# Kernel tuning notes

Measured on AMD Instinct MI355X. Metric: run time of the kernel, lower is better.

## Reference

```python
import jax, jax.numpy as jnp
import numpy as np

SEQ_LEN, BATCH, NUM_GROUPS, GROUP = 12, 512, 16, 32
H, E, MLP, BOTTLE, PRE = 128, 64, 1024, 1024, 512


def _pool_net(h, pos, num_groups, Wp, bp, W1, b1, W2, b2):
    # PoolHiddenNet: for each scene group, pairwise relative positions -> MLP -> max over neighbors
    B = h.shape[0]
    G = B // num_groups
    hg = h.reshape(num_groups, G, -1)          # (NG, G, H)
    pg = pos.reshape(num_groups, G, 2)         # (NG, G, 2)
    rel = pg[:, None, :, :] - pg[:, :, None, :]  # [g,i,j] = pos_j - pos_i
    emb = rel @ Wp.T + bp                      # (NG, G, G, E)
    hj = jnp.broadcast_to(hg[:, None, :, :], (num_groups, G, G, hg.shape[-1]))
    feats = jnp.concatenate([emb, hj], axis=-1)  # (NG, G, G, E+H)
    x = jax.nn.relu(feats @ W1.T + b1)         # (NG, G, G, 512)
    x = jax.nn.relu(x @ W2.T + b2)             # (NG, G, G, 1024)
    return x.max(axis=2).reshape(B, -1)        # max over neighbors j


def setup_inputs() -> dict:
    key = jax.random.key(0)
    ks = jax.random.split(key, 24)
    s = 0.05
    starts = np.arange(NUM_GROUPS, dtype=np.int64) * GROUP
    seq_start_end = jnp.asarray(np.stack([starts, starts + GROUP], axis=1))
    return {
        "last_pos": jax.random.normal(ks[0], (BATCH, 2), jnp.float32),
        "last_pos_rel": jax.random.normal(ks[1], (BATCH, 2), jnp.float32),
        "hh": jax.random.normal(ks[2], (1, BATCH, H), jnp.float32),
        "ch": jax.random.normal(ks[3], (1, BATCH, H), jnp.float32),
        "pred_traj_rel": jax.random.normal(ks[4], (SEQ_LEN, BATCH, 2), jnp.float32),
        "seq_start_end": seq_start_end,
        # LSTM (torch layout: gates ordered i,f,g,o)
        "W_ih": jax.random.normal(ks[5], (4 * H, E), jnp.float32) * s,
        "W_hh": jax.random.normal(ks[6], (4 * H, H), jnp.float32) * s,
        "b_ih": jax.random.normal(ks[7], (4 * H,), jnp.float32) * s,
        "b_hh": jax.random.normal(ks[8], (4 * H,), jnp.float32) * s,
        # spatial_embedding Linear(2, E)
        "Wse": jax.random.normal(ks[9], (E, 2), jnp.float32) * s,
        "bse": jax.random.normal(ks[10], (E,), jnp.float32) * s,
        # hidden2pos Linear(H, 2)
        "Wpos": jax.random.normal(ks[11], (2, H), jnp.float32) * s,
        "bpos": jax.random.normal(ks[12], (2,), jnp.float32) * s,
        # pool_net spatial_embedding Linear(2, E)
        "Wp": jax.random.normal(ks[13], (E, 2), jnp.float32) * s,
        "bp": jax.random.normal(ks[14], (E,), jnp.float32) * s,
        # pool_net mlp_pre_pool: [E+H, 512, BOTTLE], relu after each linear
        "W1": jax.random.normal(ks[15], (PRE, E + H), jnp.float32) * s,
        "b1": jax.random.normal(ks[16], (PRE,), jnp.float32) * s,
        "W2": jax.random.normal(ks[17], (BOTTLE, PRE), jnp.float32) * s,
        "b2": jax.random.normal(ks[18], (BOTTLE,), jnp.float32) * s,
        # decoder mlp: [H+BOTTLE, MLP, H], relu after each linear
        "Wm1": jax.random.normal(ks[19], (MLP, H + BOTTLE), jnp.float32) * s,
        "bm1": jax.random.normal(ks[20], (MLP,), jnp.float32) * s,
        "Wm2": jax.random.normal(ks[21], (H, MLP), jnp.float32) * s,
        "bm2": jax.random.normal(ks[22], (H,), jnp.float32) * s,
    }


def reference(last_pos, last_pos_rel, hh, ch, pred_traj_rel, seq_start_end,
              W_ih, W_hh, b_ih, b_hh, Wse, bse, Wpos, bpos,
              Wp, bp, W1, b1, W2, b2, Wm1, bm1, Wm2, bm2):
    num_groups = seq_start_end.shape[0]
    h0, c0 = hh[0], ch[0]
    dec_in0 = last_pos_rel @ Wse.T + bse

    def step(carry, gt_rel):
        last_pos_c, h, c, dec_in, loss = carry
        # single-layer LSTM cell (torch gate order i,f,g,o)
        gates = dec_in @ W_ih.T + b_ih + h @ W_hh.T + b_hh
        i, f, g, o = jnp.split(gates, 4, axis=-1)
        c = jax.nn.sigmoid(f) * c + jax.nn.sigmoid(i) * jnp.tanh(g)
        h = jax.nn.sigmoid(o) * jnp.tanh(c)
        rel_pos = h @ Wpos.T + bpos
        curr_pos = rel_pos + last_pos_c
        # pool every timestep + mlp back down to h_dim, replaces hidden state
        pool_h = _pool_net(h, curr_pos, num_groups, Wp, bp, W1, b1, W2, b2)
        dh = jnp.concatenate([h, pool_h], axis=1)
        dh = jax.nn.relu(dh @ Wm1.T + bm1)
        h = jax.nn.relu(dh @ Wm2.T + bm2)
        # training mode: teacher forcing + MSE loss
        loss = loss + jnp.mean((rel_pos - gt_rel) ** 2)
        dec_in = gt_rel @ Wse.T + bse
        return (curr_pos, h, c, dec_in, loss), rel_pos

    init = (last_pos, h0, c0, dec_in0, jnp.float32(0.0))
    (_, _, _, _, loss), pred_traj = jax.lax.scan(step, init, pred_traj_rel)
    return pred_traj, loss
```

## Files before the change

kernel.cpp:

```cpp
#include <hip/hip_runtime.h>
#include <math.h>

#define BATCH 512
#define NG 16
#define GSZ 32
#define H 128
#define E 64
#define PRE 512
#define BOT 1024
#define MLPD 1024
#define SEQ 12
#define AK 1152

typedef __attribute__((ext_vector_type(8))) short bf16x8;
typedef __attribute__((ext_vector_type(4))) float f32x4;

union bf8pack { ushort s[8]; uint4 v; };

__device__ __forceinline__ unsigned short f2bf(float f) {
    unsigned u = __float_as_uint(f);
    u += 0x7FFF + ((u >> 16) & 1);
    return (unsigned short)(u >> 16);
}

__device__ __forceinline__ uint4 pack8(const float* s) {
    float4 a = *(const float4*)s, b = *(const float4*)(s + 4);
    bf8pack o;
    o.s[0] = f2bf(a.x); o.s[1] = f2bf(a.y); o.s[2] = f2bf(a.z); o.s[3] = f2bf(a.w);
    o.s[4] = f2bf(b.x); o.s[5] = f2bf(b.y); o.s[6] = f2bf(b.z); o.s[7] = f2bf(b.w);
    return o.v;
}

#define GLB(p) ((const __attribute__((address_space(1))) unsigned int*)(p))
#define LDS(p) ((__attribute__((address_space(3))) unsigned int*)(p))

#define U0 ((BOT * PRE) / 8)
#define U1 ((MLPD * AK) / 8)
#define U2 ((H * MLPD) / 8)
#define U3 ((PRE * H) / 8)
#define U4 (PRE)
#define U5 ((BATCH * H) / 4)
#define U5b ((BATCH * H) / 8)
#define U6 (BATCH * 2)
#define U7 ((512 * 128) / 8)
#define U8 (512)
#define PREP_TOT (U0 + U1 + U2 + U3 + U4 + U5 + U5b + U6 + U7 + U8 + 1)

__global__ void prep_kernel(
    const float* __restrict__ W2, const float* __restrict__ Wm1,
    const float* __restrict__ Wm2, const float* __restrict__ W1,
    const float* __restrict__ Wp, const float* __restrict__ bp, const float* __restrict__ b1,
    const float* __restrict__ ch, const float* __restrict__ hh, const float* __restrict__ last_pos,
    const float* __restrict__ Wih, const float* __restrict__ Whh,
    const float* __restrict__ bih, const float* __restrict__ bhh,
    const float* __restrict__ Wse, const float* __restrict__ bse,
    unsigned short* __restrict__ W2pk, unsigned short* __restrict__ Wm1pk,
    unsigned short* __restrict__ Wm2pk, unsigned short* __restrict__ W1pk,
    float* __restrict__ Wcx, float* __restrict__ Wcy, float* __restrict__ biash,
    float* __restrict__ cbuf, unsigned short* __restrict__ Ahpk, float* __restrict__ pos,
    unsigned short* __restrict__ Whpk,
    float* __restrict__ Wx0, float* __restrict__ Wx1, float* __restrict__ bx,
    float* __restrict__ loss)
{
    long idx = (long)blockIdx.x * 256 + threadIdx.x;
    if (idx < U0) {
        int u = (int)idx;
        int lane = u & 63, rest = u >> 6;
        int ksg = rest & 15, cg = rest >> 4;
        int col = cg * 16 + (lane & 15);
        int kk = ksg * 32 + (lane >> 4) * 8;
        *(uint4*)&W2pk[(size_t)u * 8] = pack8(&W2[(size_t)col * PRE + kk]);
        return;
    }
    idx -= U0;
    if (idx < U1) {
        int u = (int)idx;
        int lane = u & 63, rest = u >> 6;
        int ksg = rest % 36, cg = rest / 36;
        int col = cg * 16 + (lane & 15);
        int k = ksg * 32 + (lane >> 4) * 8;
        *(uint4*)&Wm1pk[(size_t)u * 8] = pack8(&Wm1[(size_t)col * AK + k]);
        return;
    }
    idx -= U1;
    if (idx < U2) {
        int u = (int)idx;
        int lane = u & 63, rest = u >> 6;
        int ksg = rest & 31, cg = rest >> 5;
        int col = cg * 16 + (lane & 15);
        int k = ksg * 32 + (lane >> 4) * 8;
        *(uint4*)&Wm2pk[(size_t)u * 8] = pack8(&Wm2[(size_t)col * MLPD + k]);
        return;
    }
    idx -= U2;
    if (idx < U3) {
        int u = (int)idx;
        int l16 = u & 15, quad = (u >> 4) & 3, nt = (u >> 6) & 3, ks = (u >> 8) & 3, w = u >> 10;
        int col = w * 64 + nt * 16 + l16;
        int k = ks * 32 + quad * 8;
        *(uint4*)&W1pk[(size_t)u * 8] = pack8(&W1[col * 192 + E + k]);
        return;
    }
    idx -= U3;
    if (idx < U4) {
        int p = (int)idx;
        float sx = 0.f, sy = 0.f, sb = 0.f;
#pragma unroll 8
        for (int e = 0; e < E; ++e) {
            float w = W1[p * 192 + e];
            sx += w * Wp[e * 2 + 0];
            sy += w * Wp[e * 2 + 1];
            sb += w * bp[e];
        }
        Wcx[p] = sx; Wcy[p] = sy; biash[p] = b1[p] + sb;
        return;
    }
    idx -= U4;
    if (idx < U5) { ((float4*)cbuf)[idx] = ((const float4*)ch)[idx]; return; }
    idx -= U5;
    if (idx < U5b) {
        int u = (int)idx;
        int lane = u & 63, rest = u >> 6;
        int ks = rest & 3, rowtile = rest >> 2;
        int row = rowtile * 16 + (lane & 15);
        int k = ks * 32 + (lane >> 4) * 8;
        *(uint4*)&Ahpk[(size_t)u * 8] = pack8(&hh[(size_t)row * H + k]);
        return;
    }
    idx -= U5b;
    if (idx < U6) { pos[idx] = last_pos[idx]; return; }
    idx -= U6;
    if (idx < U7) {
        int u = (int)idx;
        int l16 = u & 15, quad = (u >> 4) & 3, ks = (u >> 6) & 3, w = (u >> 8) & 7, g = u >> 11;
        int col = g * 128 + w * 16 + l16;
        int k = ks * 32 + quad * 8;
        *(uint4*)&Whpk[(size_t)u * 8] = pack8(&Whh[(size_t)col * H + k]);
        return;
    }
    idx -= U7;
    if (idx < U8) {
        int u = (int)idx;
        float sx = 0.f, sy = 0.f, sb = 0.f;
#pragma unroll 8
        for (int e = 0; e < E; ++e) {
            float w = Wih[u * E + e];
            sx += w * Wse[e * 2 + 0];
            sy += w * Wse[e * 2 + 1];
            sb += w * bse[e];
        }
        Wx0[u] = sx; Wx1[u] = sy; bx[u] = sb + bih[u] + bhh[u];
        return;
    }
    idx -= U8;
    if (idx == 0) *loss = 0.0f;
}

__device__ __forceinline__ void lstm_body(
    int s, int r0, int tid, int lane, int w, int quad, int l16,
    unsigned short* hmb , unsigned short* hnb, float* hnf, float* lred,
    const float* relin, const float* gt,
    const unsigned short* Whpk,
    const float* Wx0, const float* Wx1, const float* bx,
    const float* Wpos, const float* bpos,
    const unsigned short* W1pk, const float* biash,
    float* cbuf, unsigned short* Abf, float* Hpartf,
    float* pos, float* traj, float* loss)
{
    constexpr int LDHB = 136;
    constexpr int LDHF = 129;

    f32x4 acc[4];
#pragma unroll
    for (int g4 = 0; g4 < 4; ++g4) acc[g4] = (f32x4)0.f;
#pragma unroll
    for (int ks = 0; ks < 4; ++ks) {
        bf16x8 af = *(const bf16x8*)&hmb[l16 * LDHB + ks * 32 + quad * 8];
#pragma unroll
        for (int gate = 0; gate < 4; ++gate) {
            bf16x8 bf = *(const bf16x8*)&Whpk[((size_t)((gate * 8 + w) * 4 + ks) * 64 + lane) * 8];
            acc[gate] = __builtin_amdgcn_mfma_f32_16x16x32_bf16(af, bf, acc[gate], 0, 0, 0);
        }
    }

    {
        int u = w * 16 + l16;
        float wx0[4], wx1[4], bxv[4];
#pragma unroll
        for (int gate = 0; gate < 4; ++gate) {
            int col = gate * 128 + u;
            wx0[gate] = Wx0[col]; wx1[gate] = Wx1[col]; bxv[gate] = bx[col];
        }
#pragma unroll
        for (int r = 0; r < 4; ++r) {
            int row = quad * 4 + r;
            int b = r0 + row;
            float rx = relin[b * 2 + 0], ry = relin[b * 2 + 1];
            float i_ = acc[0][r] + rx * wx0[0] + ry * wx1[0] + bxv[0];
            float f_ = acc[1][r] + rx * wx0[1] + ry * wx1[1] + bxv[1];
            float g_ = acc[2][r] + rx * wx0[2] + ry * wx1[2] + bxv[2];
            float o_ = acc[3][r] + rx * wx0[3] + ry * wx1[3] + bxv[3];
            float ig = 1.0f / (1.0f + expf(-i_));
            float fg = 1.0f / (1.0f + expf(-f_));
            float gg = tanhf(g_);
            float og = 1.0f / (1.0f + expf(-o_));
            float c = fg * cbuf[(size_t)b * H + u] + ig * gg;
            cbuf[(size_t)b * H + u] = c;
            float h = og * tanhf(c);
            hnb[row * LDHB + u] = f2bf(h);
            hnf[row * LDHF + u] = h;
            Abf[(size_t)b * AK + u] = f2bf(h);
        }
    }
    __syncthreads();

    if (s < SEQ - 1) {
        f32x4 acc2[4];
#pragma unroll
        for (int nt = 0; nt < 4; ++nt) acc2[nt] = (f32x4)0.f;
#pragma unroll
        for (int ks = 0; ks < 4; ++ks) {
            bf16x8 af = *(const bf16x8*)&hnb[l16 * LDHB + ks * 32 + quad * 8];
#pragma unroll
            for (int nt = 0; nt < 4; ++nt) {
                bf16x8 bfr = *(const bf16x8*)&W1pk[((size_t)((w * 4 + ks) * 4 + nt) * 64 + lane) * 8];
                acc2[nt] = __builtin_amdgcn_mfma_f32_16x16x32_bf16(af, bfr, acc2[nt], 0, 0, 0);
            }
        }
#pragma unroll
        for (int nt = 0; nt < 4; ++nt) {
            int col = w * 64 + nt * 16 + l16;
            float bv = biash[col];
#pragma unroll
            for (int r = 0; r < 4; ++r) {
                int row = quad * 4 + r;
                Hpartf[(size_t)(r0 + row) * PRE + col] = acc2[nt][r] + bv;
            }
        }
    }

    {
        int row = tid >> 5, o = (tid >> 4) & 1, seg = tid & 15;
        const float* wr = Wpos + o * H + seg * 8;
        const float* hr = &hnf[row * LDHF + seg * 8];
        float acc3 = 0.f;
#pragma unroll
        for (int k = 0; k < 8; ++k) acc3 += wr[k] * hr[k];
        acc3 += __shfl_xor(acc3, 1);
        acc3 += __shfl_xor(acc3, 2);
        acc3 += __shfl_xor(acc3, 4);
        acc3 += __shfl_xor(acc3, 8);
        acc3 += bpos[o];
        int b = r0 + row;
        float d = acc3 - gt[b * 2 + o];
        if (seg == 0) {
            float lp = pos[b * 2 + o];
            pos[b * 2 + o] = acc3 + lp;
            traj[b * 2 + o] = acc3;
        }
        float part = (seg == 0) ? d * d : 0.f;
        part += __shfl_xor(part, 16);
        part += __shfl_xor(part, 32);
        if (lane == 0) lred[w] = part;
        __syncthreads();
        if (tid == 0) {
            float s2 = 0.f;
#pragma unroll
            for (int i = 0; i < 8; ++i) s2 += lred[i];
            atomicAdd(loss, s2 * (1.0f / 1024.0f));
        }
    }
}

#define LROWS 16
__global__ __launch_bounds__(512) void lstm_hpart(
    const float* __restrict__ relin, const float* __restrict__ gt,
    const unsigned short* __restrict__ Whpk,
    const float* __restrict__ Wx0, const float* __restrict__ Wx1, const float* __restrict__ bx,
    const float* __restrict__ Wpos, const float* __restrict__ bpos,
    const unsigned short* __restrict__ W1pk, const float* __restrict__ biash,
    const unsigned short* __restrict__ Ahpk, float* __restrict__ cbuf,
    unsigned short* __restrict__ Abf, float* __restrict__ Hpartf,
    float* __restrict__ pos, float* __restrict__ traj, float* __restrict__ loss)
{
    constexpr int LDHB = 136;
    constexpr int LDHF = 129;
    __shared__ __align__(16) unsigned short hmb[LROWS * LDHB];
    __shared__ __align__(16) unsigned short hnb[LROWS * LDHB];
    __shared__ float hnf[LROWS * LDHF];
    __shared__ float lred[8];
    const int blk = blockIdx.x, tid = threadIdx.x;
    const int lane = tid & 63, w = tid >> 6;
    const int quad = lane >> 4, l16 = lane & 15;

    for (int e2 = tid; e2 < LROWS * H / 8; e2 += 512) {
        int lane2 = e2 & 63, ks = e2 >> 6;
        int row = lane2 & 15, k = ks * 32 + (lane2 >> 4) * 8;
        *(uint4*)&hmb[row * LDHB + k] = *(const uint4*)&Ahpk[((size_t)(blk * 4 + ks) * 64 + lane2) * 8];
    }
    __syncthreads();

    lstm_body(0, blk * LROWS, tid, lane, w, quad, l16, hmb, hnb, hnf, lred,
              relin, gt, Whpk, Wx0, Wx1, bx, Wpos, bpos, W1pk, biash,
              cbuf, Abf, Hpartf, pos, traj, loss);
}

__global__ __launch_bounds__(512) void mlp2_lstm(
    int s,
    const unsigned short* __restrict__ dhpk,
    const unsigned short* __restrict__ Wm2pk, const float* __restrict__ bm2,
    const float* __restrict__ relin, const float* __restrict__ gt,
    const unsigned short* __restrict__ Whpk,
    const float* __restrict__ Wx0, const float* __restrict__ Wx1, const float* __restrict__ bx,
    const float* __restrict__ Wpos, const float* __restrict__ bpos,
    const unsigned short* __restrict__ W1pk, const float* __restrict__ biash,
    float* __restrict__ cbuf,
    unsigned short* __restrict__ Abf, float* __restrict__ Hpartf,
    float* __restrict__ pos, float* __restrict__ traj, float* __restrict__ loss)
{
    constexpr int LDHB = 136;
    constexpr int LDHF = 129;
    __shared__ __align__(16) unsigned short hmb[LROWS * LDHB];
    __shared__ __align__(16) unsigned short hnb[LROWS * LDHB];
    __shared__ float hnf[LROWS * LDHF];
    __shared__ float lred[8];
    const int blk = blockIdx.x, tid = threadIdx.x;
    const int lane = tid & 63, w = tid >> 6;
    const int quad = lane >> 4, l16 = lane & 15;

    f32x4 acc0 = (f32x4)0.f;
#pragma unroll 8
    for (int ki = 0; ki < 32; ++ki) {
        bf16x8 af = *(const bf16x8*)&dhpk[((size_t)(blk * 32 + ki) * 64 + lane) * 8];
        bf16x8 bf = *(const bf16x8*)&Wm2pk[((size_t)(w * 32 + ki) * 64 + lane) * 8];
        acc0 = __builtin_amdgcn_mfma_f32_16x16x32_bf16(af, bf, acc0, 0, 0, 0);
    }
    {
        int u = w * 16 + l16;
        float bv = bm2[u];
#pragma unroll
        for (int r = 0; r < 4; ++r)
            hmb[(quad * 4 + r) * LDHB + u] = f2bf(fmaxf(acc0[r] + bv, 0.f));
    }
    __syncthreads();

    lstm_body(s, blk * LROWS, tid, lane, w, quad, l16, hmb, hnb, hnf, lred,
              relin, gt, Whpk, Wx0, Wx1, bx, Wpos, bpos, W1pk, biash,
              cbuf, Abf, Hpartf, pos, traj, loss);
}

template <int BM, int BN, int KW, int NW, int MODE>
__global__ __launch_bounds__(256) void gemm_splitk_pk(
    const unsigned short* __restrict__ A, int lda,
    const unsigned short* __restrict__ Bpk, int K,
    const float* __restrict__ bias,
    float* __restrict__ Cf, unsigned short* __restrict__ Cb, int ldc)
{
    constexpr int MT = BM / 16;
    constexpr int NT = BN / (16 * NW);
    constexpr int ABUF = KW * BM * 64;
    __shared__ __align__(16) unsigned short As[2 * ABUF];
    __shared__ float red[KW * BM * BN];
    int tid = threadIdx.x;
    int lane = tid & 63, w = tid >> 6;
    int kslice = w / NW, nslice = w % NW;
    int gtid = tid & (NW * 64 - 1);
    int quad = lane >> 4, l16 = lane & 15;
    int m0 = blockIdx.y * BM, n0 = blockIdx.x * BN;
    const int KC = K / KW;
    const int NK = KC / 64;
    const int KSGT = K >> 5;
    const int cgbase = (n0 + nslice * (BN / NW)) >> 4;

    auto STAGE = [&](int ki, int bo) {
        int kb = kslice * KC + ki * 64;
#pragma unroll
        for (int u = 0; u < BM / (8 * NW); ++u) {
            int c = u * NW * 64 + gtid;
            __builtin_amdgcn_global_load_lds(
                GLB(A + (size_t)(m0 + (c >> 3)) * lda + kb + (c & 7) * 8),
                LDS(&As[bo + kslice * BM * 64 + c * 8]), 16, 0, 0);
        }
    };

    f32x4 acc[MT][NT];
#pragma unroll
    for (int mt = 0; mt < MT; ++mt)
#pragma unroll
        for (int nt = 0; nt < NT; ++nt) acc[mt][nt] = (f32x4)0.f;

    STAGE(0, 0);
    for (int ki = 0; ki < NK; ++ki) {
        int bo = (ki & 1) * ABUF;
        int kgbase = (kslice * KC + ki * 64) >> 5;
        __syncthreads();
#pragma unroll
        for (int ks = 0; ks < 2; ++ks) {
            bf16x8 af[MT], bfr[NT];
#pragma unroll
            for (int mt = 0; mt < MT; ++mt)
                af[mt] = *(const bf16x8*)&As[bo + kslice * BM * 64 + (mt * 16 + l16) * 64 + ks * 32 + quad * 8];
#pragma unroll
            for (int nt = 0; nt < NT; ++nt)
                bfr[nt] = *(const bf16x8*)&Bpk[((size_t)((cgbase + nt) * KSGT + kgbase + ks) * 64 + lane) * 8];
#pragma unroll
            for (int mt = 0; mt < MT; ++mt)
#pragma unroll
                for (int nt = 0; nt < NT; ++nt)
                    acc[mt][nt] = __builtin_amdgcn_mfma_f32_16x16x32_bf16(af[mt], bfr[nt], acc[mt][nt], 0, 0, 0);
        }
        if (ki + 1 < NK) STAGE(ki + 1, ((ki + 1) & 1) * ABUF);
    }

#pragma unroll
    for (int mt = 0; mt < MT; ++mt)
#pragma unroll
    for (int nt = 0; nt < NT; ++nt) {
#pragma unroll
        for (int r = 0; r < 4; ++r) {
            int row = mt * 16 + quad * 4 + r;
            int col = nslice * (BN / NW) + nt * 16 + l16;
            red[kslice * BM * BN + row * BN + col] = acc[mt][nt][r];
        }
    }
    __syncthreads();

#pragma unroll
    for (int o = 0; o < BM * BN / 256; ++o) {
        int e = o * 256 + tid;
        int row = e / BN, col = e % BN;
        float s = 0.f;
#pragma unroll
        for (int k = 0; k < KW; ++k) s += red[k * BM * BN + e];
        float v = fmaxf(s + bias[n0 + col], 0.f);
        if (MODE == 1) {
            Cb[(size_t)(m0 + row) * ldc + n0 + col] = f2bf(v);
        } else if (MODE == 2) {
            Cf[(size_t)(m0 + row) * ldc + n0 + col] = v;
        } else {
            int gr = m0 + row, gc = n0 + col;
            int rowtile = gr >> 4, l16p = gr & 15;
            int ksv = gc >> 5, quadp = (gc >> 3) & 3, ep = gc & 7;
            int lanep = quadp * 16 + l16p;
            Cb[((size_t)(rowtile * (ldc >> 5) + ksv) * 64 + lanep) * 8 + ep] = f2bf(v);
        }
    }
}

__global__ __launch_bounds__(512) void pool_fused(
    const float* __restrict__ Hpartf, const float* __restrict__ pos,
    const float* __restrict__ Wcx, const float* __restrict__ Wcy,
    const unsigned short* __restrict__ W2pk,
    const float* __restrict__ b2, unsigned short* __restrict__ Abf)
{
    constexpr int LDA = 72;
    constexpr int ASZ = 128 * LDA;
    __shared__ __align__(16) unsigned short As[2 * ASZ];
    const int tid = threadIdx.x;
    const int lane = tid & 63, w = tid >> 6;
    const int quad = lane >> 4, l16 = lane & 15;
    const int n_tile = blockIdx.x, m_tile = blockIdx.y;
    const int g = m_tile >> 3, iq = m_tile & 7;
    const int n0 = n_tile * 512;

    const int brow = tid >> 2;
    const int k8 = (tid & 3) * 16;
    const int bi = iq * 4 + (brow >> 5), bj = brow & 31;
    const float rx = pos[(g * GSZ + bj) * 2 + 0] - pos[(g * GSZ + bi) * 2 + 0];
    const float ry = pos[(g * GSZ + bj) * 2 + 1] - pos[(g * GSZ + bi) * 2 + 1];
    const float* hrow = &Hpartf[(size_t)(g * GSZ + bj) * PRE];

    auto BUILD = [&](int k0i, unsigned short* dst) {
        const int k0 = k0i * 64;
        const float4* hp = (const float4*)(hrow + k0 + k8);
        const float4* wx = (const float4*)(Wcx + k0 + k8);
        const float4* wy = (const float4*)(Wcy + k0 + k8);
        bf8pack o[2];
#pragma unroll
        for (int q = 0; q < 2; ++q) {
            float4 ha = hp[q * 2], hb = hp[q * 2 + 1];
            float4 xa = wx[q * 2], xb = wx[q * 2 + 1];
            float4 ya = wy[q * 2], yb = wy[q * 2 + 1];
            o[q].s[0] = f2bf(fmaxf(ha.x + rx * xa.x + ry * ya.x, 0.f));
            o[q].s[1] = f2bf(fmaxf(ha.y + rx * xa.y + ry * ya.y, 0.f));
            o[q].s[2] = f2bf(fmaxf(ha.z + rx * xa.z + ry * ya.z, 0.f));
            o[q].s[3] = f2bf(fmaxf(ha.w + rx * xa.w + ry * ya.w, 0.f));
            o[q].s[4] = f2bf(fmaxf(hb.x + rx * xb.x + ry * yb.x, 0.f));
            o[q].s[5] = f2bf(fmaxf(hb.y + rx * xb.y + ry * yb.y, 0.f));
            o[q].s[6] = f2bf(fmaxf(hb.z + rx * xb.z + ry * yb.z, 0.f));
            o[q].s[7] = f2bf(fmaxf(hb.w + rx * xb.w + ry * yb.w, 0.f));
        }
        *(uint4*)&dst[brow * LDA + k8] = o[0].v;
        *(uint4*)&dst[brow * LDA + k8 + 8] = o[1].v;
    };

    f32x4 acc[8][4];
#pragma unroll
    for (int mt = 0; mt < 8; ++mt)
#pragma unroll
        for (int nt = 0; nt < 4; ++nt) acc[mt][nt] = (f32x4)0.f;

    BUILD(0, As);
    for (int k0i = 0; k0i < 8; ++k0i) {
        unsigned short* cur = As + (k0i & 1) * ASZ;
        __syncthreads();
        __builtin_amdgcn_s_setprio(1);
#pragma unroll
        for (int ks = 0; ks < 2; ++ks) {
            bf16x8 bfr[4];
#pragma unroll
            for (int nt = 0; nt < 4; ++nt) {
                int cg = n_tile * 32 + w * 4 + nt;
                int ksg = k0i * 2 + ks;
                bfr[nt] = *(const bf16x8*)&W2pk[((size_t)(cg * 16 + ksg) * 64 + lane) * 8];
            }
#pragma unroll
            for (int mt = 0; mt < 8; ++mt) {
                bf16x8 af = *(const bf16x8*)&cur[(mt * 16 + l16) * LDA + ks * 32 + quad * 8];
#pragma unroll
                for (int nt = 0; nt < 4; ++nt)
                    acc[mt][nt] = __builtin_amdgcn_mfma_f32_16x16x32_bf16(af, bfr[nt], acc[mt][nt], 0, 0, 0);
            }
        }
        __builtin_amdgcn_s_setprio(0);
        if (k0i < 7) BUILD(k0i + 1, As + ((k0i + 1) & 1) * ASZ);
    }

#pragma unroll
    for (int il = 0; il < 4; ++il)
#pragma unroll
    for (int nt = 0; nt < 4; ++nt) {
        float u = -1e30f;
#pragma unroll
        for (int p = 0; p < 2; ++p)
#pragma unroll
            for (int r = 0; r < 4; ++r) u = fmaxf(u, acc[il * 2 + p][nt][r]);
        u = fmaxf(u, __shfl_xor(u, 16));
        u = fmaxf(u, __shfl_xor(u, 32));
        if (lane < 16) {
            int col = n0 + w * 64 + nt * 16 + l16;
            int gu = m_tile * 4 + il;
            Abf[(size_t)gu * AK + H + col] = f2bf(fmaxf(u + b2[col], 0.f));
        }
    }
}

extern "C" void kernel_launch(void* const* d_in, const int* in_sizes, int n_in,
                              void* d_out, int out_size, void* d_ws, size_t ws_size,
                              hipStream_t stream)
{
    const float* last_pos     = (const float*)d_in[0];
    const float* last_pos_rel = (const float*)d_in[1];
    const float* hh           = (const float*)d_in[2];
    const float* ch           = (const float*)d_in[3];
    const float* ptr_rel      = (const float*)d_in[4];
    const float* Wih  = (const float*)d_in[6];
    const float* Whh  = (const float*)d_in[7];
    const float* bih  = (const float*)d_in[8];
    const float* bhh  = (const float*)d_in[9];
    const float* Wse  = (const float*)d_in[10];
    const float* bse  = (const float*)d_in[11];
    const float* Wpos = (const float*)d_in[12];
    const float* bpos = (const float*)d_in[13];
    const float* Wp   = (const float*)d_in[14];
    const float* bp   = (const float*)d_in[15];
    const float* W1   = (const float*)d_in[16];
    const float* b1   = (const float*)d_in[17];
    const float* W2   = (const float*)d_in[18];
    const float* b2   = (const float*)d_in[19];
    const float* Wm1  = (const float*)d_in[20];
    const float* bm1  = (const float*)d_in[21];
    const float* Wm2  = (const float*)d_in[22];
    const float* bm2  = (const float*)d_in[23];

    float* ws     = (float*)d_ws;
    unsigned short* Ahpk = (unsigned short*)ws;
    float* cbuf   = ws + BATCH * H;
    float* pos    = cbuf + BATCH * H;
    float* Hpartf = pos + 1024;
    float* Wcx    = Hpartf + BATCH * PRE;
    float* Wcy    = Wcx + PRE;
    float* biash  = Wcy + PRE;
    float* bx     = biash + PRE;
    float* Wx0    = bx + 512;
    float* Wx1    = Wx0 + 512;
    unsigned short* ub    = (unsigned short*)(Wx1 + 512);
    unsigned short* Abf   = ub;
    unsigned short* dhpk  = Abf + (size_t)BATCH * AK;
    unsigned short* W2pk  = dhpk + (size_t)BATCH * MLPD;
    unsigned short* Wm1pk = W2pk + (size_t)BOT * PRE;
    unsigned short* Wm2pk = Wm1pk + (size_t)MLPD * AK;
    unsigned short* W1pk  = Wm2pk + (size_t)H * MLPD;
    unsigned short* Whpk  = W1pk + (size_t)PRE * H;

    float* out  = (float*)d_out;
    float* loss = out + SEQ * BATCH * 2;

    prep_kernel<<<(PREP_TOT + 255) / 256, 256, 0, stream>>>(
        W2, Wm1, Wm2, W1, Wp, bp, b1, ch, hh, last_pos, Wih, Whh, bih, bhh, Wse, bse,
        W2pk, Wm1pk, Wm2pk, W1pk, Wcx, Wcy, biash, cbuf, Ahpk, pos, Whpk, Wx0, Wx1, bx, loss);

    lstm_hpart<<<BATCH / LROWS, 512, 0, stream>>>(
        last_pos_rel, ptr_rel, Whpk, Wx0, Wx1, bx, Wpos, bpos, W1pk, biash,
        Ahpk, cbuf, Abf, Hpartf, pos, out, loss);

    for (int t = 0; t < SEQ - 1; t++) {
        pool_fused<<<dim3(2, 128), 512, 0, stream>>>(Hpartf, pos, Wcx, Wcy, W2pk, b2, Abf);
        gemm_splitk_pk<64, 32, 2, 2, 3><<<dim3(MLPD / 32, BATCH / 64), 256, 0, stream>>>(
            Abf, AK, Wm1pk, AK, bm1, nullptr, dhpk, MLPD);
        mlp2_lstm<<<BATCH / LROWS, 512, 0, stream>>>(
            t + 1, dhpk, Wm2pk, bm2,
            ptr_rel + t * BATCH * 2, ptr_rel + (t + 1) * BATCH * 2,
            Whpk, Wx0, Wx1, bx, Wpos, bpos, W1pk, biash,
            cbuf, Abf, Hpartf, pos, out + (t + 1) * BATCH * 2, loss);
    }
}
```

Before: 645.0 us.

## Halve pool_fused M-tile to double grid, pad split-K reduction buffer

The pool_fused kernel now handles 64 pair-rows (2 agents × 32 neighbours) per block instead of 128. Its grid doubles to 512 blocks and each block uses half the accumulators and LDS. This is meant to fill more CUs and cut register pressure, at the cost of re-reading the W2 fragments twice as often. Separately, the split-K reduction buffer in gemm_splitk_pk gets a +1 row padding to avoid LDS bank conflicts, in exchange for more index arithmetic in the reduction.

```diff
diff --git a/kernel.cpp b/kernel.cpp
--- a/kernel.cpp
+++ b/kernel.cpp
@@ -359,8 +359,9 @@
     constexpr int MT = BM / 16;
     constexpr int NT = BN / (16 * NW);
     constexpr int ABUF = KW * BM * 64;
+    constexpr int BNP = BN + 1;
     __shared__ __align__(16) unsigned short As[2 * ABUF];
-    __shared__ float red[KW * BM * BN];
+    __shared__ float red[KW * BM * BNP];
     int tid = threadIdx.x;
     int lane = tid & 63, w = tid >> 6;
     int kslice = w / NW, nslice = w % NW;
@@ -420,7 +421,7 @@
         for (int r = 0; r < 4; ++r) {
             int row = mt * 16 + quad * 4 + r;
             int col = nslice * (BN / NW) + nt * 16 + l16;
-            red[kslice * BM * BN + row * BN + col] = acc[mt][nt][r];
+            red[kslice * BM * BNP + row * BNP + col] = acc[mt][nt][r];
         }
     }
     __syncthreads();
@@ -431,7 +432,7 @@
         int row = e / BN, col = e % BN;
         float s = 0.f;
 #pragma unroll
-        for (int k = 0; k < KW; ++k) s += red[k * BM * BN + e];
+        for (int k = 0; k < KW; ++k) s += red[k * BM * BNP + row * BNP + col];
         float v = fmaxf(s + bias[n0 + col], 0.f);
         if (MODE == 1) {
             Cb[(size_t)(m0 + row) * ldc + n0 + col] = f2bf(v);
@@ -454,49 +455,45 @@
     const float* __restrict__ b2, unsigned short* __restrict__ Abf)
 {
     constexpr int LDA = 72;
-    constexpr int ASZ = 128 * LDA;
+    constexpr int ASZ = 64 * LDA;
     __shared__ __align__(16) unsigned short As[2 * ASZ];
     const int tid = threadIdx.x;
     const int lane = tid & 63, w = tid >> 6;
     const int quad = lane >> 4, l16 = lane & 15;
-    const int n_tile = blockIdx.x, m_tile = blockIdx.y;
-    const int g = m_tile >> 3, iq = m_tile & 7;
+    const int n_tile = blockIdx.x, m_tile2 = blockIdx.y;
+    const int g = m_tile2 >> 4, iq2 = m_tile2 & 15;
     const int n0 = n_tile * 512;
 
-    const int brow = tid >> 2;
-    const int k8 = (tid & 3) * 16;
-    const int bi = iq * 4 + (brow >> 5), bj = brow & 31;
+    const int brow = tid >> 3;
+    const int k8 = (tid & 7) * 8;
+    const int bi = iq2 * 2 + (brow >> 5), bj = brow & 31;
     const float rx = pos[(g * GSZ + bj) * 2 + 0] - pos[(g * GSZ + bi) * 2 + 0];
     const float ry = pos[(g * GSZ + bj) * 2 + 1] - pos[(g * GSZ + bi) * 2 + 1];
     const float* hrow = &Hpartf[(size_t)(g * GSZ + bj) * PRE];
 
     auto BUILD = [&](int k0i, unsigned short* dst) {
         const int k0 = k0i * 64;
-        const float4* hp = (const float4*)(hrow + k0 + k8);
-        const float4* wx = (const float4*)(Wcx + k0 + k8);
-        const float4* wy = (const float4*)(Wcy + k0 + k8);
-        bf8pack o[2];
-#pragma unroll
-        for (int q = 0; q < 2; ++q) {
-            float4 ha = hp[q * 2], hb = hp[q * 2 + 1];
-            float4 xa = wx[q * 2], xb = wx[q * 2 + 1];
-            float4 ya = wy[q * 2], yb = wy[q * 2 + 1];
-            o[q].s[0] = f2bf(fmaxf(ha.x + rx * xa.x + ry * ya.x, 0.f));
-            o[q].s[1] = f2bf(fmaxf(ha.y + rx * xa.y + ry * ya.y, 0.f));
-            o[q].s[2] = f2bf(fmaxf(ha.z + rx * xa.z + ry * ya.z, 0.f));
-            o[q].s[3] = f2bf(fmaxf(ha.w + rx * xa.w + ry * ya.w, 0.f));
-            o[q].s[4] = f2bf(fmaxf(hb.x + rx * xb.x + ry * yb.x, 0.f));
-            o[q].s[5] = f2bf(fmaxf(hb.y + rx * xb.y + ry * yb.y, 0.f));
-            o[q].s[6] = f2bf(fmaxf(hb.z + rx * xb.z + ry * yb.z, 0.f));
-            o[q].s[7] = f2bf(fmaxf(hb.w + rx * xb.w + ry * yb.w, 0.f));
-        }
-        *(uint4*)&dst[brow * LDA + k8] = o[0].v;
-        *(uint4*)&dst[brow * LDA + k8 + 8] = o[1].v;
+        const float* hp = hrow + k0 + k8;
+        const float* wx = Wcx + k0 + k8;
+        const float* wy = Wcy + k0 + k8;
+        float4 ha = *(const float4*)hp, hb = *(const float4*)(hp + 4);
+        float4 xa = *(const float4*)wx, xb = *(const float4*)(wx + 4);
+        float4 ya = *(const float4*)wy, yb = *(const float4*)(wy + 4);
+        bf8pack o;
+        o.s[0] = f2bf(fmaxf(ha.x + rx * xa.x + ry * ya.x, 0.f));
+        o.s[1] = f2bf(fmaxf(ha.y + rx * xa.y + ry * ya.y, 0.f));
+        o.s[2] = f2bf(fmaxf(ha.z + rx * xa.z + ry * ya.z, 0.f));
+        o.s[3] = f2bf(fmaxf(ha.w + rx * xa.w + ry * ya.w, 0.f));
+        o.s[4] = f2bf(fmaxf(hb.x + rx * xb.x + ry * yb.x, 0.f));
+        o.s[5] = f2bf(fmaxf(hb.y + rx * xb.y + ry * yb.y, 0.f));
+        o.s[6] = f2bf(fmaxf(hb.z + rx * xb.z + ry * yb.z, 0.f));
+        o.s[7] = f2bf(fmaxf(hb.w + rx * xb.w + ry * yb.w, 0.f));
+        *(uint4*)&dst[brow * LDA + k8] = o.v;
     };
 
-    f32x4 acc[8][4];
-#pragma unroll
-    for (int mt = 0; mt < 8; ++mt)
+    f32x4 acc[4][4];
+#pragma unroll
+    for (int mt = 0; mt < 4; ++mt)
 #pragma unroll
         for (int nt = 0; nt < 4; ++nt) acc[mt][nt] = (f32x4)0.f;
 
@@ -515,7 +512,7 @@
                 bfr[nt] = *(const bf16x8*)&W2pk[((size_t)(cg * 16 + ksg) * 64 + lane) * 8];
             }
 #pragma unroll
-            for (int mt = 0; mt < 8; ++mt) {
+            for (int mt = 0; mt < 4; ++mt) {
                 bf16x8 af = *(const bf16x8*)&cur[(mt * 16 + l16) * LDA + ks * 32 + quad * 8];
 #pragma unroll
                 for (int nt = 0; nt < 4; ++nt)
@@ -527,7 +524,7 @@
     }
 
 #pragma unroll
-    for (int il = 0; il < 4; ++il)
+    for (int il = 0; il < 2; ++il)
 #pragma unroll
     for (int nt = 0; nt < 4; ++nt) {
         float u = -1e30f;
@@ -539,7 +536,7 @@
         u = fmaxf(u, __shfl_xor(u, 32));
         if (lane < 16) {
             int col = n0 + w * 64 + nt * 16 + l16;
-            int gu = m_tile * 4 + il;
+            int gu = m_tile2 * 2 + il;
             Abf[(size_t)gu * AK + H + col] = f2bf(fmaxf(u + b2[col], 0.f));
         }
     }
@@ -605,7 +602,7 @@
         Ahpk, cbuf, Abf, Hpartf, pos, out, loss);
 
     for (int t = 0; t < SEQ - 1; t++) {
-        pool_fused<<<dim3(2, 128), 512, 0, stream>>>(Hpartf, pos, Wcx, Wcy, W2pk, b2, Abf);
+        pool_fused<<<dim3(2, 256), 512, 0, stream>>>(Hpartf, pos, Wcx, Wcy, W2pk, b2, Abf);
         gemm_splitk_pk<64, 32, 2, 2, 3><<<dim3(MLPD / 32, BATCH / 64), 256, 0, stream>>>(
             Abf, AK, Wm1pk, AK, bm1, nullptr, dhpk, MLPD);
         mlp2_lstm<<<BATCH / LROWS, 512, 0, stream>>>(
```

Result: faster. 575.0 us, median of 2 (-10.8%).
